# Performance work log

Measured on AMD Instinct MI355X. Metric: run time of the kernel, lower is better.

## Reference

```python
import jax, jax.numpy as jnp
import numpy as np

B, CIN, H, W = 4, 256, 56, 56
COUT, K = 256, 3
STRIDE, PAD, OG = 1, 1, 1
KK = K * K


def setup_inputs() -> dict:
    key = jax.random.key(0)
    k1, k2, k3, k4 = jax.random.split(key, 4)
    x = jax.random.normal(k1, (B, CIN, H, W), jnp.float32)
    # deformable conv weight [Cout, Cin/groups, K, K]
    weight = jax.random.normal(k2, (COUT, CIN, K, K), jnp.float32) * 0.05
    # offset-predicting 3x3 conv: 2*OG*K*K output channels (small init -> modest offsets)
    off_w = jax.random.normal(k3, (2 * OG * KK, CIN, 3, 3), jnp.float32) * 0.01
    off_b = jax.random.normal(k4, (2 * OG * KK,), jnp.float32) * 0.01
    return {"x": x, "weight": weight, "off_w": off_w, "off_b": off_b}


def _deform_conv(x, weight, off_w, off_b):
    Bn, C, Hh, Ww = x.shape
    # offset = param_generator(x): 3x3 conv, stride 1, pad 1
    offset = jax.lax.conv_general_dilated(
        x, off_w, window_strides=(1, 1), padding=((1, 1), (1, 1)),
        dimension_numbers=("NCHW", "OIHW", "NCHW")) + off_b[None, :, None, None]
    Ho = (Hh + 2 * PAD - K) // STRIDE + 1
    Wo = (Ww + 2 * PAD - K) // STRIDE + 1
    # torchvision layout: [B, OG, KK, (dy,dx), Ho, Wo]
    off = offset.reshape(Bn, OG, KK, 2, Ho, Wo)

    kh = jnp.arange(KK) // K
    kw = jnp.arange(KK) % K
    base_y = (jnp.arange(Ho) * STRIDE - PAD)[None, :, None] + kh[:, None, None]  # [KK,Ho,1]
    base_x = (jnp.arange(Wo) * STRIDE - PAD)[None, None, :] + kw[:, None, None]  # [KK,1,Wo]
    py = base_y[None, None].astype(x.dtype) + off[:, :, :, 0]  # [B,OG,KK,Ho,Wo]
    px = base_x[None, None].astype(x.dtype) + off[:, :, :, 1]

    Cg = C // OG
    xg = x.reshape(Bn, OG, Cg, Hh * Ww)

    def gather(yc, xc, wgt):
        # zero-padded bilinear corner: out-of-bounds samples contribute 0
        valid = (yc >= 0) & (yc < Hh) & (xc >= 0) & (xc < Ww)
        idx = (jnp.clip(yc, 0, Hh - 1) * Ww + jnp.clip(xc, 0, Ww - 1)).reshape(Bn, OG, 1, -1)
        v = jnp.take_along_axis(xg, idx, axis=3)            # [B,OG,Cg,KK*Ho*Wo]
        w = (wgt * valid.astype(wgt.dtype)).reshape(Bn, OG, 1, -1)
        return v * w

    y0 = jnp.floor(py).astype(jnp.int32)
    x0 = jnp.floor(px).astype(jnp.int32)
    ty = py - y0
    tx = px - x0
    sampled = (gather(y0,     x0,     (1 - ty) * (1 - tx))
             + gather(y0,     x0 + 1, (1 - ty) * tx)
             + gather(y0 + 1, x0,     ty * (1 - tx))
             + gather(y0 + 1, x0 + 1, ty * tx))
    sampled = sampled.reshape(Bn, C, KK, Ho, Wo)
    # weighted accumulation: implicit GEMM over (Cin, KK)
    return jnp.einsum("bikhw,oik->bohw", sampled, weight.reshape(COUT, C, KK))


def reference(x, weight, off_w, off_b):
    return _deform_conv(x, weight, off_w, off_b)
```

## Files before the change

kernel.cpp:

```cpp
#include <hip/hip_runtime.h>
#include <hip/hip_bf16.h>

#define B_N   4
#define CIN_  256
#define HH_   56
#define WW_   56
#define COUT_ 256
#define KK_   9
#define HW_   3136
#define KDIM  2304
#define NOFF  (B_N*18*HW_)
#define NOUT  (B_N*COUT_*HW_)

typedef __attribute__((ext_vector_type(8))) short short8;
typedef __attribute__((ext_vector_type(4))) float float4v;

__device__ __forceinline__ short f2bf_bits(float v) {
    union { __hip_bfloat16 h; short s; } u;
    u.h = __float2bfloat16(v);
    return u.s;
}
__device__ __forceinline__ float bfbits2f(short s) {
    union { unsigned u; float f; } u2;
    u2.u = ((unsigned)(unsigned short)s) << 16;
    return u2.f;
}

#define NB_AT  2304
#define NB_XT  784
#define NB_OW3 288
__global__ __launch_bounds__(256) void k_front(const float* __restrict__ x,
                                               const float* __restrict__ wgt,
                                               const float* __restrict__ ow,
                                               short* __restrict__ At,
                                               short* __restrict__ xTb,
                                               short* __restrict__ owT3) {
    __shared__ float tile[64][65];
    int bx = blockIdx.x;
    int t = threadIdx.x;
    if (bx < NB_AT) {
        int i = bx*256 + t;
        int o = i / KDIM; int r = i % KDIM;
        int kk = r >> 8;  int ci = r & 255;
        At[i] = f2bf_bits(wgt[(size_t)(o*CIN_ + ci)*9 + kk]);
        return;
    }
    if (bx < NB_AT + NB_XT) {
        int g = bx - NB_AT;
        int b = g / 196; int r = g % 196;
        int c0 = (r / 49) * 64; int p0 = (r % 49) * 64;
        int tp = t & 63;  int tc = t >> 6;
        #pragma unroll
        for (int i = 0; i < 16; ++i) {
            int ci = tc*16 + i;
            tile[ci][tp] = x[((size_t)b*CIN_ + c0 + ci)*HW_ + p0 + tp];
        }
        __syncthreads();
        #pragma unroll
        for (int i = 0; i < 16; ++i) {
            int p = tc*16 + i;
            xTb[((size_t)b*HW_ + p0 + p)*CIN_ + c0 + tp] = f2bf_bits(tile[tp][p]);
        }
        return;
    }
    {
        int i = (bx - NB_AT - NB_XT)*256 + t;
        int c = i / KDIM; int r = i % KDIM;
        int kk = r >> 8;  int ci = r & 255;
        owT3[i] = (c < 18) ? f2bf_bits(ow[(size_t)(c*CIN_ + ci)*9 + kk]) : 0;
    }
}

__global__ __launch_bounds__(256) void k_offgemm(const short* __restrict__ owT3,
                                                 const short* __restrict__ xTb,
                                                 float* __restrict__ pOff2) {
    __shared__ short sA[32*64];
    __shared__ short sB[64*64];
    __shared__ int   sP2[3*64];
    int t = threadIdx.x;
    int posb = blockIdx.x * 64;
    int b    = blockIdx.y;
    int ks   = blockIdx.z;
    int kt0  = ks * 768;
    int kend = kt0 + 768;

    for (int e = t; e < 3*64; e += 256) {
        int kk = ks*3 + (e >> 6); int row = e & 63;
        int pos = posb + row;
        int h = pos / WW_, w = pos % WW_;
        int yy = h + kk/3 - 1, xx = w + kk%3 - 1;
        bool v = (yy >= 0) && (yy < HH_) && (xx >= 0) && (xx < WW_);
        sP2[e] = v ? (yy*WW_ + xx) : -1;
    }
    __syncthreads();

    int arow = t >> 3,  aq  = t & 7;
    int brow = t >> 2,  bqc = (t & 3) * 2;

    int wv = t >> 6;
    int wm = (wv >> 1) * 16;
    int wn = (wv & 1) * 32;
    int lane = t & 63;
    int lm = lane & 15;
    int qd = lane >> 4;

    float4v acc[2];
    acc[0] = (float4v)(0.f); acc[1] = (float4v)(0.f);

    const short* gA = owT3 + (size_t)arow*KDIM + aq*8;
    const short* xb = xTb + (size_t)b*HW_*CIN_;

    short* wA = sA + (((arow >> 4)*8 + aq)*16 + ((arow + 2*aq) & 15))*8;
    short* wB[2];
    #pragma unroll
    for (int j = 0; j < 2; ++j) {
        int qq = bqc + j;
        wB[j] = sB + (((brow >> 4)*8 + qq)*16 + ((brow + 2*qq) & 15))*8;
    }

    short8 pa, pb[2];
    const short8 zero8 = (short8)(0);
    pa = *(const short8*)(gA + kt0);
    {
        int p2 = sP2[brow];
        #pragma unroll
        for (int j = 0; j < 2; ++j) {
            int ci0 = (kt0 & 255) + (bqc + j)*8;
            pb[j] = (p2 >= 0) ? *(const short8*)(xb + (size_t)p2*CIN_ + ci0) : zero8;
        }
    }

    for (int kt = kt0; kt < kend; kt += 64) {
        __syncthreads();
        *(short8*)wA = pa;
        #pragma unroll
        for (int j = 0; j < 2; ++j) *(short8*)wB[j] = pb[j];
        __syncthreads();
        int kt2 = kt + 64;
        if (kt2 < kend) {
            pa = *(const short8*)(gA + kt2);
            int kkl = (kt2 >> 8) - ks*3;
            int p2 = sP2[kkl*64 + brow];
            int cb = kt2 & 255;
            #pragma unroll
            for (int j = 0; j < 2; ++j) {
                int ci0 = cb + (bqc + j)*8;
                pb[j] = (p2 >= 0) ? *(const short8*)(xb + (size_t)p2*CIN_ + ci0) : zero8;
            }
        }
        #pragma unroll
        for (int kss = 0; kss < 2; ++kss) {
            int qe = kss*4 + qd;
            int sw = (lm + 2*qe) & 15;
            short8 af, bf[2];
            af = *(short8*)(sA + ((((wm>>4))*8 + qe)*16 + sw)*8);
            #pragma unroll
            for (int j = 0; j < 2; ++j)
                bf[j] = *(short8*)(sB + ((((wn>>4) + j)*8 + qe)*16 + sw)*8);
            #pragma unroll
            for (int j = 0; j < 2; ++j)
                acc[j] = __builtin_amdgcn_mfma_f32_16x16x32_bf16(
                             af, bf[j], acc[j], 0, 0, 0);
        }
    }

    float* pbase = pOff2 + (size_t)ks*NOFF;
    #pragma unroll
    for (int j = 0; j < 2; ++j) {
        int col = posb + wn + j*16 + lm;
        #pragma unroll
        for (int r = 0; r < 4; ++r) {
            int c = wm + qd*4 + r;
            if (c < 18)
                pbase[((size_t)(b*18 + c))*HW_ + col] = acc[j][r];
        }
    }
}

__global__ __launch_bounds__(256) void k_gemm(const short* __restrict__ At,
                                              const short* __restrict__ xTb,
                                              const float* __restrict__ pOff2,
                                              const float* __restrict__ ob,
                                              float* __restrict__ pout) {
    __shared__ short sA[128*64];
    __shared__ short sB[64*64];
    __shared__ int4   sPI[3*64];
    __shared__ float4 sPW[3*64];
    int t = threadIdx.x;

    int idx = blockIdx.x;
    int xcd = idx & 7;
    int b   = xcd & 3;
    int q   = (idx >> 3)*2 + (xcd >> 2);
    int m0   = (q & 1) * 128;
    int r2   = q >> 1;
    int posb = (r2 % 49) * 64;
    int ks   = r2 / 49;
    int kt0  = ks * 768;
    int kend = kt0 + 768;

    for (int e = t; e < 3*64; e += 256) {
        int kk = ks*3 + (e >> 6); int pl = e & 63;
        int pos = posb + pl;
        int h = pos / WW_, w = pos % WW_;
        size_t oy = (size_t)(b*18 + 2*kk    )*HW_ + pos;
        size_t ox = (size_t)(b*18 + 2*kk + 1)*HW_ + pos;
        float dy = ob[2*kk], dx = ob[2*kk + 1];
        #pragma unroll
        for (int s = 0; s < 3; ++s) {
            dy += pOff2[(size_t)s*NOFF + oy];
            dx += pOff2[(size_t)s*NOFF + ox];
        }
        float py = (float)(h - 1 + kk/3) + dy;
        float px = (float)(w - 1 + kk%3) + dx;
        float y0f = floorf(py), x0f = floorf(px);
        int y0 = (int)y0f, x0 = (int)x0f;
        float ty = py - y0f, tx = px - x0f;
        bool vy0 = (y0   >= 0) && (y0   < HH_);
        bool vy1 = (y0+1 >= 0) && (y0+1 < HH_);
        bool vx0 = (x0   >= 0) && (x0   < WW_);
        bool vx1 = (x0+1 >= 0) && (x0+1 < WW_);
        int y0c = min(max(y0,   0), HH_-1), y1c = min(max(y0+1, 0), HH_-1);
        int x0c = min(max(x0,   0), WW_-1), x1c = min(max(x0+1, 0), WW_-1);
        sPI[e] = make_int4(y0c*WW_+x0c, y0c*WW_+x1c, y1c*WW_+x0c, y1c*WW_+x1c);
        sPW[e] = make_float4((vy0 && vx0) ? (1.f-ty)*(1.f-tx) : 0.f,
                             (vy0 && vx1) ? (1.f-ty)*tx       : 0.f,
                             (vy1 && vx0) ? ty*(1.f-tx)       : 0.f,
                             (vy1 && vx1) ? ty*tx             : 0.f);
    }
    __syncthreads();

    int arow = t >> 1,  aqc = (t & 1) * 4;
    int brow = t >> 2,  bqc = (t & 3) * 2;

    int wv = t >> 6;
    int wm = (wv >> 1) * 64;
    int wn = (wv & 1) * 32;
    int lane = t & 63;
    int lm = lane & 15;
    int qd = lane >> 4;

    float4v acc[4][2];
    #pragma unroll
    for (int i = 0; i < 4; ++i)
        #pragma unroll
        for (int j = 0; j < 2; ++j) acc[i][j] = (float4v)(0.f);

    const short* gA = At + (size_t)(m0 + arow)*KDIM + aqc*8;
    const short* xb = xTb + (size_t)b*HW_*CIN_;

    short* wA[4]; short* wB[2];
    #pragma unroll
    for (int j = 0; j < 4; ++j) {
        int qq = aqc + j;
        wA[j] = sA + (((arow >> 4)*8 + qq)*16 + ((arow + 2*qq) & 15))*8;
    }
    #pragma unroll
    for (int j = 0; j < 2; ++j) {
        int qq = bqc + j;
        wB[j] = sB + (((brow >> 4)*8 + qq)*16 + ((brow + 2*qq) & 15))*8;
    }

    short8 pa[4], cg[2][4];
    float4 bwv;
    #pragma unroll
    for (int j = 0; j < 4; ++j) pa[j] = *(const short8*)(gA + kt0 + j*8);
    {
        int4 id = sPI[brow]; bwv = sPW[brow];
        #pragma unroll
        for (int j = 0; j < 2; ++j) {
            int ci0 = (bqc + j)*8;
            cg[j][0] = *(const short8*)(xb + (size_t)id.x*CIN_ + ci0);
            cg[j][1] = *(const short8*)(xb + (size_t)id.y*CIN_ + ci0);
            cg[j][2] = *(const short8*)(xb + (size_t)id.z*CIN_ + ci0);
            cg[j][3] = *(const short8*)(xb + (size_t)id.w*CIN_ + ci0);
        }
    }

    for (int kt = kt0; kt < kend; kt += 64) {
        short8 pk[2];
        #pragma unroll
        for (int j = 0; j < 2; ++j) {
            float f[8];
            #pragma unroll
            for (int e = 0; e < 8; ++e)
                f[e] = bwv.x*bfbits2f(cg[j][0][e]) + bwv.y*bfbits2f(cg[j][1][e])
                     + bwv.z*bfbits2f(cg[j][2][e]) + bwv.w*bfbits2f(cg[j][3][e]);
            union { short8 s8; __hip_bfloat162 h2[4]; } pu;
            #pragma unroll
            for (int e2 = 0; e2 < 4; ++e2)
                pu.h2[e2] = __float22bfloat162_rn(make_float2(f[2*e2], f[2*e2+1]));
            pk[j] = pu.s8;
        }
        __syncthreads();
        #pragma unroll
        for (int j = 0; j < 4; ++j) *(short8*)wA[j] = pa[j];
        #pragma unroll
        for (int j = 0; j < 2; ++j) *(short8*)wB[j] = pk[j];
        __syncthreads();
        int kt2 = kt + 64;
        if (kt2 < kend) {
            #pragma unroll
            for (int j = 0; j < 4; ++j) pa[j] = *(const short8*)(gA + kt2 + j*8);
            int kkl = (kt2 >> 8) - ks*3;
            int4 id = sPI[kkl*64 + brow]; bwv = sPW[kkl*64 + brow];
            int cb = kt2 & 255;
            #pragma unroll
            for (int j = 0; j < 2; ++j) {
                int ci0 = cb + (bqc + j)*8;
                cg[j][0] = *(const short8*)(xb + (size_t)id.x*CIN_ + ci0);
                cg[j][1] = *(const short8*)(xb + (size_t)id.y*CIN_ + ci0);
                cg[j][2] = *(const short8*)(xb + (size_t)id.z*CIN_ + ci0);
                cg[j][3] = *(const short8*)(xb + (size_t)id.w*CIN_ + ci0);
            }
        }
        #pragma unroll
        for (int kss = 0; kss < 2; ++kss) {
            int qe = kss*4 + qd;
            int sw = (lm + 2*qe) & 15;
            short8 af[4], bf[2];
            #pragma unroll
            for (int i = 0; i < 4; ++i)
                af[i] = *(short8*)(sA + ((((wm>>4) + i)*8 + qe)*16 + sw)*8);
            #pragma unroll
            for (int j = 0; j < 2; ++j)
                bf[j] = *(short8*)(sB + ((((wn>>4) + j)*8 + qe)*16 + sw)*8);
            #pragma unroll
            for (int i = 0; i < 4; ++i)
                #pragma unroll
                for (int j = 0; j < 2; ++j)
                    acc[i][j] = __builtin_amdgcn_mfma_f32_16x16x32_bf16(
                                    af[i], bf[j], acc[i][j], 0, 0, 0);
        }
    }

    float* pbase = pout + (size_t)ks*NOUT;
    #pragma unroll
    for (int i = 0; i < 4; ++i)
        #pragma unroll
        for (int j = 0; j < 2; ++j) {
            int col = posb + wn + j*16 + lm;
            #pragma unroll
            for (int r = 0; r < 4; ++r) {
                int m = m0 + wm + i*16 + qd*4 + r;
                pbase[((size_t)b*COUT_ + m)*HW_ + col] = acc[i][j][r];
            }
        }
}

__global__ __launch_bounds__(256) void k_oreduce(const float* __restrict__ pout,
                                                 float* __restrict__ out) {
    int i = blockIdx.x*256 + threadIdx.x;
    if (i >= NOUT/4) return;
    float4 a = ((const float4*)pout)[i];
    float4 b = ((const float4*)(pout + NOUT))[i];
    float4 c = ((const float4*)(pout + 2*(size_t)NOUT))[i];
    float4 r;
    r.x = a.x + b.x + c.x;  r.y = a.y + b.y + c.y;
    r.z = a.z + b.z + c.z;  r.w = a.w + b.w + c.w;
    ((float4*)out)[i] = r;
}

extern "C" void kernel_launch(void* const* d_in, const int* in_sizes, int n_in,
                              void* d_out, int out_size, void* d_ws, size_t ws_size,
                              hipStream_t stream) {
    const float* x   = (const float*)d_in[0];
    const float* wgt = (const float*)d_in[1];
    const float* ow  = (const float*)d_in[2];
    const float* ob  = (const float*)d_in[3];
    float* out = (float*)d_out;

    char* ws = (char*)d_ws;
    short* At    = (short*)ws;
    short* xTb   = (short*)(ws + 1179648);
    short* owT3  = (short*)(ws + 7602176);
    float* pOff2 = (float*)(ws + 7749632);
    float* pout  = (float*)(ws + 10459136);

    k_front  <<<dim3(NB_AT + NB_XT + NB_OW3), 256, 0, stream>>>(x, wgt, ow, At, xTb, owT3);
    k_offgemm<<<dim3(49, 4, 3),               256, 0, stream>>>(owT3, xTb, pOff2);
    k_gemm   <<<dim3(1176),                   256, 0, stream>>>(At, xTb, pOff2, ob, pout);
    k_oreduce<<<dim3(NOUT/4/256),             256, 0, stream>>>(pout, out);
}
```

Baseline: 133.1 us.

## Widen GEMM block tile to all 256 output channels to avoid duplicate gathers

```diff
diff --git a/kernel.cpp b/kernel.cpp
--- a/kernel.cpp
+++ b/kernel.cpp
@@ -182,18 +182,15 @@
                                               const float* __restrict__ pOff2,
                                               const float* __restrict__ ob,
                                               float* __restrict__ pout) {
-    __shared__ short sA[128*64];
+    __shared__ short sA[256*64];
     __shared__ short sB[64*64];
     __shared__ int4   sPI[3*64];
     __shared__ float4 sPW[3*64];
     int t = threadIdx.x;
 
     int idx = blockIdx.x;
-    int xcd = idx & 7;
-    int b   = xcd & 3;
-    int q   = (idx >> 3)*2 + (xcd >> 2);
-    int m0   = (q & 1) * 128;
-    int r2   = q >> 1;
+    int b    = idx & 3;
+    int r2   = idx >> 2;
     int posb = (r2 % 49) * 64;
     int ks   = r2 / 49;
     int kt0  = ks * 768;
@@ -230,41 +227,38 @@
     }
     __syncthreads();
 
-    int arow = t >> 1,  aqc = (t & 1) * 4;
     int brow = t >> 2,  bqc = (t & 3) * 2;
 
     int wv = t >> 6;
-    int wm = (wv >> 1) * 64;
-    int wn = (wv & 1) * 32;
+    int wm = wv * 64;
     int lane = t & 63;
     int lm = lane & 15;
     int qd = lane >> 4;
 
-    float4v acc[4][2];
+    float4v acc[4][4];
     #pragma unroll
     for (int i = 0; i < 4; ++i)
         #pragma unroll
-        for (int j = 0; j < 2; ++j) acc[i][j] = (float4v)(0.f);
-
-    const short* gA = At + (size_t)(m0 + arow)*KDIM + aqc*8;
+        for (int j = 0; j < 4; ++j) acc[i][j] = (float4v)(0.f);
+
+    const short* gA = At + (size_t)t*KDIM;
     const short* xb = xTb + (size_t)b*HW_*CIN_;
 
-    short* wA[4]; short* wB[2];
-    #pragma unroll
-    for (int j = 0; j < 4; ++j) {
-        int qq = aqc + j;
-        wA[j] = sA + (((arow >> 4)*8 + qq)*16 + ((arow + 2*qq) & 15))*8;
-    }
+    int wAo[8];
+    #pragma unroll
+    for (int j = 0; j < 8; ++j)
+        wAo[j] = (((t >> 4)*8 + j)*16 + ((t + 2*j) & 15))*8;
+    short* wB[2];
     #pragma unroll
     for (int j = 0; j < 2; ++j) {
         int qq = bqc + j;
         wB[j] = sB + (((brow >> 4)*8 + qq)*16 + ((brow + 2*qq) & 15))*8;
     }
 
-    short8 pa[4], cg[2][4];
+    short8 pa[8], cg[2][4];
     float4 bwv;
     #pragma unroll
-    for (int j = 0; j < 4; ++j) pa[j] = *(const short8*)(gA + kt0 + j*8);
+    for (int j = 0; j < 8; ++j) pa[j] = *(const short8*)(gA + kt0 + j*8);
     {
         int4 id = sPI[brow]; bwv = sPW[brow];
         #pragma unroll
@@ -277,6 +271,7 @@
         }
     }
 
+    #pragma unroll 1
     for (int kt = kt0; kt < kend; kt += 64) {
         short8 pk[2];
         #pragma unroll
@@ -294,14 +289,14 @@
         }
         __syncthreads();
         #pragma unroll
-        for (int j = 0; j < 4; ++j) *(short8*)wA[j] = pa[j];
+        for (int j = 0; j < 8; ++j) *(short8*)(sA + wAo[j]) = pa[j];
         #pragma unroll
         for (int j = 0; j < 2; ++j) *(short8*)wB[j] = pk[j];
         __syncthreads();
         int kt2 = kt + 64;
         if (kt2 < kend) {
             #pragma unroll
-            for (int j = 0; j < 4; ++j) pa[j] = *(const short8*)(gA + kt2 + j*8);
+            for (int j = 0; j < 8; ++j) pa[j] = *(const short8*)(gA + kt2 + j*8);
             int kkl = (kt2 >> 8) - ks*3;
             int4 id = sPI[kkl*64 + brow]; bwv = sPW[kkl*64 + brow];
             int cb = kt2 & 255;
@@ -318,17 +313,17 @@
         for (int kss = 0; kss < 2; ++kss) {
             int qe = kss*4 + qd;
             int sw = (lm + 2*qe) & 15;
-            short8 af[4], bf[2];
+            short8 af[4], bf[4];
             #pragma unroll
             for (int i = 0; i < 4; ++i)
                 af[i] = *(short8*)(sA + ((((wm>>4) + i)*8 + qe)*16 + sw)*8);
             #pragma unroll
-            for (int j = 0; j < 2; ++j)
-                bf[j] = *(short8*)(sB + ((((wn>>4) + j)*8 + qe)*16 + sw)*8);
+            for (int j = 0; j < 4; ++j)
+                bf[j] = *(short8*)(sB + (((j)*8 + qe)*16 + sw)*8);
             #pragma unroll
             for (int i = 0; i < 4; ++i)
                 #pragma unroll
-                for (int j = 0; j < 2; ++j)
+                for (int j = 0; j < 4; ++j)
                     acc[i][j] = __builtin_amdgcn_mfma_f32_16x16x32_bf16(
                                     af[i], bf[j], acc[i][j], 0, 0, 0);
         }
@@ -338,11 +333,11 @@
     #pragma unroll
     for (int i = 0; i < 4; ++i)
         #pragma unroll
-        for (int j = 0; j < 2; ++j) {
-            int col = posb + wn + j*16 + lm;
+        for (int j = 0; j < 4; ++j) {
+            int col = posb + j*16 + lm;
             #pragma unroll
             for (int r = 0; r < 4; ++r) {
-                int m = m0 + wm + i*16 + qd*4 + r;
+                int m = wm + i*16 + qd*4 + r;
                 pbase[((size_t)b*COUT_ + m)*HW_ + col] = acc[i][j][r];
             }
         }
@@ -379,6 +374,6 @@
 
     k_front  <<<dim3(NB_AT + NB_XT + NB_OW3), 256, 0, stream>>>(x, wgt, ow, At, xTb, owT3);
     k_offgemm<<<dim3(49, 4, 3),               256, 0, stream>>>(owT3, xTb, pOff2);
-    k_gemm   <<<dim3(1176),                   256, 0, stream>>>(At, xTb, pOff2, ob, pout);
+    k_gemm   <<<dim3(588),                    256, 0, stream>>>(At, xTb, pOff2, ob, pout);
     k_oreduce<<<dim3(NOUT/4/256),             256, 0, stream>>>(pout, out);
 }
```

New measurement: 154.7 us. 1.16x slower.
